# Kernel tuning notes

Measured on AMD Instinct MI355X. Metric: run time of the kernel, lower is better.

The kernel has to match this reference:

```python
import jax, jax.numpy as jnp
import numpy as np

# ---- LIF constants (LIFParams defaults assumed; see notes) ----
SLOPE = 5.0      # surrogate_slope from module
TAU = 20.0
V_REST = -65.0
V_RESET = -65.0
V_TH = -50.0
DT = 1.0

@jax.custom_vjp
def spike(x):
    return (x >= 0).astype(x.dtype)

def _spike_fwd(x):
    return spike(x), x

def _spike_bwd(x, g):
    # fast-sigmoid surrogate gradient
    return (g / (SLOPE * jnp.abs(x) + 1.0) ** 2,)

spike.defvjp(_spike_fwd, _spike_bwd)

def lif_step(v, cur):
    v_new = v + (DT / TAU) * ((V_REST - v) + cur)
    s = spike(v_new - V_TH)
    v_out = v_new - s * (v_new - V_RESET)  # soft reset, grad flows via surrogate
    return v_out, s


def setup_inputs() -> dict:
    key = jax.random.key(0)
    ks = jax.random.split(key, 6)
    B, T = 128, 256
    sizes = [1024, 1024, 1024, 512, 256, 128]  # n_input, hidden..., n_output
    out = {}
    for i in range(5):
        out[f"w{i}"] = jax.random.uniform(ks[i], (sizes[i], sizes[i + 1]), dtype=jnp.float32) * 0.1
    out["input_spikes"] = (jax.random.uniform(ks[5], (B, sizes[0], T)) < 0.2).astype(jnp.float32)
    return out


def _forward(input_spikes, w_layers):
    B, n_in, T = input_spikes.shape
    hidden = [w.shape[1] for w in w_layers[:-1]]
    n_out = w_layers[-1].shape[1]
    dtype = input_spikes.dtype

    # precompute input current for all timesteps: (T, B, H0)
    cur_in = jnp.einsum('bit,ih->tbh', input_spikes, jax.nn.relu(w_layers[0]))
    rws = [jax.nn.relu(w) for w in w_layers[1:]]  # hidden->hidden..., ->output

    v_init = tuple(jnp.full((B, h), V_REST, dtype=dtype) for h in hidden)
    s_init = tuple(jnp.zeros((B, h), dtype=dtype) for h in hidden)
    vo_init = jnp.full((B, n_out), V_REST, dtype=dtype)

    n_hidden = len(hidden)

    def step(carry, cur0):
        vs, vo, sp = carry
        new_vs, new_s = [], []
        v0, s0 = lif_step(vs[0], cur0)
        new_vs.append(v0); new_s.append(s0)
        for li in range(1, n_hidden):
            c = sp[li - 1] @ rws[li - 1]
            v, s = lif_step(vs[li], c)
            new_vs.append(v); new_s.append(s)
        co = sp[-1] @ rws[-1]          # output driven by previous-step spikes
        vo2, so = lif_step(vo, co)
        return (tuple(new_vs), vo2, tuple(new_s)), (tuple(new_s), so)

    _, (hid_T, out_T) = jax.lax.scan(step, (v_init, vo_init, s_init), cur_in)
    hidden_spikes = [jnp.transpose(h, (1, 2, 0)) for h in hid_T]   # (B, h, T)
    output_spikes = jnp.transpose(out_T, (1, 2, 0))                # (B, n_out, T)
    firing_rates = output_spikes.mean(axis=2)
    return hidden_spikes, output_spikes, firing_rates


def reference(input_spikes, w0, w1, w2, w3, w4):
    hidden_spikes, output_spikes, firing_rates = _forward(input_spikes, [w0, w1, w2, w3, w4])
    return (*hidden_spikes, output_spikes, firing_rates)
```

## Files before the change

kernel.cpp:

```cpp
#include <hip/hip_runtime.h>
#include <cstdint>

using u16 = unsigned short;
using u32 = unsigned int;
typedef __attribute__((ext_vector_type(8))) short bhalf8;
typedef __attribute__((ext_vector_type(4))) float floatx4;

__device__ __forceinline__ float bf2f(u16 u) {
  union { unsigned int i; float f; } v; v.i = ((unsigned int)u) << 16; return v.f;
}
__device__ __forceinline__ u16 f2bf(float f) {
  union { float f; unsigned int i; } v; v.f = f;
  unsigned int r = v.i + 0x7fffu + ((v.i >> 16) & 1u);
  return (u16)(r >> 16);
}

__device__ __forceinline__ void gload16(const void* g, void* l) {
  __builtin_amdgcn_global_load_lds((const __attribute__((address_space(1))) void*)g,
                                   (__attribute__((address_space(3))) void*)l, 16, 0, 0);
}

__global__ __launch_bounds__(256) void prep_all(
    const float* __restrict__ w0, const float* __restrict__ w1,
    const float* __restrict__ w2, const float* __restrict__ w3,
    const float* __restrict__ w4, const float* __restrict__ sp,
    u16* __restrict__ W0, u16* __restrict__ W1, u16* __restrict__ W2,
    u16* __restrict__ W3, u16* __restrict__ W4, u16* __restrict__ S,
    u32* __restrict__ flags) {
  const int bid = blockIdx.x;
  const int tid = threadIdx.x;
  const int tx = tid & 31, ty = tid >> 5;
  __shared__ float tile[32][33];

  if (bid == 2720) {
    if (tid < 64) flags[tid] = 0u;
    return;
  }
  if (bid > 2720) {
    const int rel = bid - 2721;
    const int b  = rel >> 8;
    const int i0 = ((rel >> 3) & 31) * 32;
    const int t0 = (rel & 7) * 32;
    const size_t I = 1024, T = 256;
#pragma unroll
    for (int r = 0; r < 4; ++r)
      tile[ty + r * 8][tx] = sp[((size_t)b * I + i0 + ty + r * 8) * T + t0 + tx];
    __syncthreads();
#pragma unroll
    for (int r = 0; r < 4; ++r)
      S[((size_t)(t0 + ty + r * 8) * 128 + b) * I + i0 + tx] = f2bf(tile[tx][ty + r * 8]);
    return;
  }

  const float* W; u16* Wt; int K, N, rel;
  if (bid < 1024)      { W = w0; Wt = W0; K = 1024; N = 1024; rel = bid; }
  else if (bid < 2048) { W = w1; Wt = W1; K = 1024; N = 1024; rel = bid - 1024; }
  else if (bid < 2560) { W = w2; Wt = W2; K = 1024; N =  512; rel = bid - 2048; }
  else if (bid < 2688) { W = w3; Wt = W3; K =  512; N =  256; rel = bid - 2560; }
  else                 { W = w4; Wt = W4; K =  256; N =  128; rel = bid - 2688; }
  const int nx = K >> 5;
  const int k0 = (rel % nx) * 32;
  const int n0 = (rel / nx) * 32;
#pragma unroll
  for (int r = 0; r < 4; ++r)
    tile[ty + r * 8][tx] = W[(size_t)(k0 + ty + r * 8) * N + n0 + tx];
  __syncthreads();
#pragma unroll
  for (int r = 0; r < 4; ++r)
    Wt[(size_t)(n0 + ty + r * 8) * K + k0 + tx] = f2bf(fmaxf(tile[tx][ty + r * 8], 0.f));
}

__global__ __launch_bounds__(256) void gemm_bf16(const u16* __restrict__ A,
                                                 const u16* __restrict__ Bt,
                                                 u16* __restrict__ C,
                                                 int K, int N,
                                                 const u32* __restrict__ flags) {
  __shared__ __align__(16) u16 As[128][64];
  __shared__ __align__(16) u16 Bs[128][64];
  const int tid  = threadIdx.x;
  const int lane = tid & 63;
  const int wave = tid >> 6;
  const int nTn  = N >> 7;
  const int chunk = (256 * nTn) >> 3;
  const int swz   = ((int)blockIdx.x & 7) * chunk + ((int)blockIdx.x >> 3);
  const int mt    = swz / nTn;
  const int nt    = swz - mt * nTn;

  if (flags && (((flags[mt >> 5] >> (mt & 31)) & 1u) == 0u)) return;

  floatx4 acc[4][4];
#pragma unroll
  for (int i = 0; i < 4; ++i)
#pragma unroll
    for (int j = 0; j < 4; ++j)
      acc[i][j] = (floatx4){0.f, 0.f, 0.f, 0.f};

  const int wm = (wave >> 1) * 64;
  const int wn = (wave & 1) * 64;
  const int fr = lane & 15;
  const int fg = lane >> 4;

  const int r_l = lane >> 3;
  const int c_l = (lane & 7) ^ r_l;

  const u16* gA = A  + (size_t)(mt * 128) * K;
  const u16* gB = Bt + (size_t)(nt * 128) * K;

  for (int kt = 0; kt < K; kt += 64) {
#pragma unroll
    for (int q = 0; q < 4; ++q) {
      const int rb0 = (wave * 4 + q) * 8;
      const int rt  = rb0 + r_l;
      gload16(gA + (size_t)rt * K + kt + c_l * 8, &As[rb0][0]);
      gload16(gB + (size_t)rt * K + kt + c_l * 8, &Bs[rb0][0]);
    }
    __syncthreads();

#pragma unroll
    for (int kk = 0; kk < 2; ++kk) {
      bhalf8 af[4], bf[4];
#pragma unroll
      for (int i = 0; i < 4; ++i) {
        const int ra = wm + i * 16 + fr;
        const int rb = wn + i * 16 + fr;
        af[i] = *(const bhalf8*)(&As[ra][((((kk << 2) | fg) ^ (ra & 7)) << 3)]);
        bf[i] = *(const bhalf8*)(&Bs[rb][((((kk << 2) | fg) ^ (rb & 7)) << 3)]);
      }
#pragma unroll
      for (int i = 0; i < 4; ++i)
#pragma unroll
        for (int j = 0; j < 4; ++j)
          acc[i][j] = __builtin_amdgcn_mfma_f32_16x16x32_bf16(af[i], bf[j], acc[i][j], 0, 0, 0);
    }
    __syncthreads();
  }

  const size_t rbase = (size_t)(mt * 128 + wm + fg * 4);
  const size_t cbase = (size_t)(nt * 128 + wn + fr);
#pragma unroll
  for (int i = 0; i < 4; ++i)
#pragma unroll
    for (int j = 0; j < 4; ++j)
#pragma unroll
      for (int r = 0; r < 4; ++r)
        C[(rbase + i * 16 + r) * (size_t)N + cbase + j * 16] = f2bf(acc[i][j][r]);
}

__global__ __launch_bounds__(256) void lif_scan(const u16* __restrict__ Cur,
                                                const u32* __restrict__ aflag,
                                                float* __restrict__ out,
                                                u16* __restrict__ sshift,
                                                u32* __restrict__ oflag,
                                                float* __restrict__ rates,
                                                int H) {
  const int gidx = blockIdx.x * 256 + threadIdx.x;
  const size_t BH = (size_t)128 * H;
  u32 fw[8];
  u32 any = 0;
#pragma unroll
  for (int w = 0; w < 8; ++w) {
    fw[w] = aflag ? aflag[w] : 0xffffffffu;
    any |= fw[w];
  }

  if (any == 0u) {
    const float4 z = {0.f, 0.f, 0.f, 0.f};
    float* base = out + (size_t)blockIdx.x * 65536 + threadIdx.x * 4;
#pragma unroll
    for (int k = 0; k < 64; ++k)
      *(float4*)(base + (size_t)k * 1024) = z;
    if (rates) rates[gidx] = 0.f;
    return;
  }

  float v = -65.f;
  float ssum = 0.f;
  if (sshift) sshift[gidx] = 0;
  float buf[16];
  for (int t0 = 0; t0 < 256; t0 += 16) {
    u32 wavemask = 0;
#pragma unroll
    for (int j = 0; j < 16; ++j) {
      const int t = t0 + j;
      const bool act = ((fw[t >> 5] >> (t & 31)) & 1u) != 0u;
      const float c  = act ? bf2f(Cur[(size_t)t * BH + gidx]) : 0.f;
      const float vn = v + 0.05f * ((-65.f - v) + c);
      const float s  = (vn >= -50.f) ? 1.f : 0.f;
      v = vn - s * (vn + 65.f);
      ssum += s;
      buf[j] = s;
      if (sshift && t < 255)
        sshift[(size_t)(t + 1) * BH + gidx] = (u16)((s != 0.f) ? 0x3F80u : 0u);
      if (oflag) {
        if (__ballot(s != 0.f) != 0ull) wavemask |= (1u << j);
      }
    }
    if (t0 == 240) wavemask &= 0x7fffu;
    if (oflag && wavemask && ((threadIdx.x & 63) == 0)) {
      const unsigned long long m = (unsigned long long)wavemask << ((t0 + 1) & 31);
      const int w = (t0 + 1) >> 5;
      if ((u32)m) atomicOr(&oflag[w], (u32)m);
      if (m >> 32) atomicOr(&oflag[w + 1], (u32)(m >> 32));
    }
    float* o = out + (size_t)gidx * 256 + t0;
#pragma unroll
    for (int q = 0; q < 4; ++q) {
      float4 wv;
      wv.x = buf[q * 4 + 0]; wv.y = buf[q * 4 + 1];
      wv.z = buf[q * 4 + 2]; wv.w = buf[q * 4 + 3];
      *(float4*)(o + q * 4) = wv;
    }
  }
  if (rates) rates[gidx] = ssum * (1.f / 256.f);
}

extern "C" void kernel_launch(void* const* d_in, const int* in_sizes, int n_in,
                              void* d_out, int out_size, void* d_ws, size_t ws_size,
                              hipStream_t stream) {
  const float* w0 = (const float*)d_in[0];
  const float* w1 = (const float*)d_in[1];
  const float* w2 = (const float*)d_in[2];
  const float* w3 = (const float*)d_in[3];
  const float* w4 = (const float*)d_in[4];
  const float* spikes = (const float*)d_in[5];

  uint8_t* ws = (uint8_t*)d_ws;
  u16* S0 = (u16*)(ws + 0);
  u16* S1 = (u16*)(ws + 67108864);
  u16* Cb = (u16*)(ws + 134217728);
  u16* W0 = (u16*)(ws + 201326592);
  u16* W1 = (u16*)(ws + 203423744);
  u16* W2 = (u16*)(ws + 205520896);
  u16* W3 = (u16*)(ws + 206569472);
  u16* W4 = (u16*)(ws + 206831616);
  u32* FL = (u32*)(ws + 206897152);
  u32* F1 = FL +  0;
  u32* F2 = FL + 16;
  u32* F3 = FL + 32;
  u32* F4 = FL + 48;

  float* out0  = (float*)d_out;
  float* out1  = out0 + 33554432;
  float* out2  = out0 + 67108864;
  float* out3  = out0 + 83886080;
  float* out4  = out0 + 92274688;
  float* rates = out0 + 96468992;

  prep_all<<<2721 + 32768, 256, 0, stream>>>(w0, w1, w2, w3, w4, spikes,
                                             W0, W1, W2, W3, W4, S0, FL);

  gemm_bf16<<<256 * 8, 256, 0, stream>>>(S0, W0, Cb, 1024, 1024, nullptr);
  lif_scan<<<512, 256, 0, stream>>>(Cb, nullptr, out0, S1, F1, nullptr, 1024);

  gemm_bf16<<<256 * 8, 256, 0, stream>>>(S1, W1, Cb, 1024, 1024, F1);
  lif_scan<<<512, 256, 0, stream>>>(Cb, F1, out1, S0, F2, nullptr, 1024);

  gemm_bf16<<<256 * 4, 256, 0, stream>>>(S0, W2, Cb, 1024, 512, F2);
  lif_scan<<<256, 256, 0, stream>>>(Cb, F2, out2, S1, F3, nullptr, 512);

  gemm_bf16<<<256 * 2, 256, 0, stream>>>(S1, W3, Cb, 512, 256, F3);
  lif_scan<<<128, 256, 0, stream>>>(Cb, F3, out3, S0, F4, nullptr, 256);

  gemm_bf16<<<256 * 1, 256, 0, stream>>>(S0, W4, Cb, 256, 128, F4);
  lif_scan<<<64, 256, 0, stream>>>(Cb, F4, out4, nullptr, nullptr, rates, 128);
}
```

Measured before the change: 752.4 us.

## Bit-pack spikes in LIF scan and write fp32 outputs coalesced via LDS

The LIF scan now keeps each thread's 256 spikes as eight 32-bit words instead of writing a float4 strip per 16 steps, where each thread wrote to its own strided 1KB row. After the scan, the words go through shared memory so groups of lanes write contiguous 128-byte segments of the (B,H,T) float output, and firing rates come from popcount. The input-spike transpose in prep now uses float4 loads and ushort4 stores. This adds an LDS buffer and a barrier, and fully unrolls the 256-step loop, which may raise register pressure and code size.

```diff
diff --git a/kernel.cpp b/kernel.cpp
--- a/kernel.cpp
+++ b/kernel.cpp
@@ -29,7 +29,6 @@
     u32* __restrict__ flags) {
   const int bid = blockIdx.x;
   const int tid = threadIdx.x;
-  const int tx = tid & 31, ty = tid >> 5;
   __shared__ float tile[32][33];
 
   if (bid == 2720) {
@@ -42,16 +41,28 @@
     const int i0 = ((rel >> 3) & 31) * 32;
     const int t0 = (rel & 7) * 32;
     const size_t I = 1024, T = 256;
-#pragma unroll
-    for (int r = 0; r < 4; ++r)
-      tile[ty + r * 8][tx] = sp[((size_t)b * I + i0 + ty + r * 8) * T + t0 + tx];
+    {
+      const int r  = tid >> 3;
+      const int c4 = (tid & 7) * 4;
+      const float4 v = *(const float4*)(sp + ((size_t)b * I + i0 + r) * T + t0 + c4);
+      tile[r][c4 + 0] = v.x; tile[r][c4 + 1] = v.y;
+      tile[r][c4 + 2] = v.z; tile[r][c4 + 3] = v.w;
+    }
     __syncthreads();
-#pragma unroll
-    for (int r = 0; r < 4; ++r)
-      S[((size_t)(t0 + ty + r * 8) * 128 + b) * I + i0 + tx] = f2bf(tile[tx][ty + r * 8]);
+    {
+      const int tr = tid >> 3;
+      const int ic = (tid & 7) * 4;
+      ushort4 o;
+      o.x = f2bf(tile[ic + 0][tr]);
+      o.y = f2bf(tile[ic + 1][tr]);
+      o.z = f2bf(tile[ic + 2][tr]);
+      o.w = f2bf(tile[ic + 3][tr]);
+      *(ushort4*)(&S[((size_t)(t0 + tr) * 128 + b) * I + i0 + ic]) = o;
+    }
     return;
   }
 
+  const int tx = tid & 31, ty = tid >> 5;
   const float* W; u16* Wt; int K, N, rel;
   if (bid < 1024)      { W = w0; Wt = W0; K = 1024; N = 1024; rel = bid; }
   else if (bid < 2048) { W = w1; Wt = W1; K = 1024; N = 1024; rel = bid - 1024; }
@@ -153,7 +164,8 @@
                                                 u32* __restrict__ oflag,
                                                 float* __restrict__ rates,
                                                 int H) {
-  const int gidx = blockIdx.x * 256 + threadIdx.x;
+  const int tid  = threadIdx.x;
+  const int gidx = blockIdx.x * 256 + tid;
   const size_t BH = (size_t)128 * H;
   u32 fw[8];
   u32 any = 0;
@@ -165,8 +177,7 @@
 
   if (any == 0u) {
     const float4 z = {0.f, 0.f, 0.f, 0.f};
-    float* base = out + (size_t)blockIdx.x * 65536 + threadIdx.x * 4;
-#pragma unroll
+    float* base = out + (size_t)blockIdx.x * 65536 + tid * 4;
     for (int k = 0; k < 64; ++k)
       *(float4*)(base + (size_t)k * 1024) = z;
     if (rates) rates[gidx] = 0.f;
@@ -174,44 +185,63 @@
   }
 
   float v = -65.f;
-  float ssum = 0.f;
+  u32 spk[8];
   if (sshift) sshift[gidx] = 0;
-  float buf[16];
-  for (int t0 = 0; t0 < 256; t0 += 16) {
-    u32 wavemask = 0;
-#pragma unroll
-    for (int j = 0; j < 16; ++j) {
+#pragma unroll
+  for (int t0c = 0; t0c < 8; ++t0c) {
+    const int t0 = t0c * 32;
+    u32 word = 0, cmask = 0;
+#pragma unroll
+    for (int j = 0; j < 32; ++j) {
       const int t = t0 + j;
       const bool act = ((fw[t >> 5] >> (t & 31)) & 1u) != 0u;
-      const float c  = act ? bf2f(Cur[(size_t)t * BH + gidx]) : 0.f;
-      const float vn = v + 0.05f * ((-65.f - v) + c);
-      const float s  = (vn >= -50.f) ? 1.f : 0.f;
-      v = vn - s * (vn + 65.f);
-      ssum += s;
-      buf[j] = s;
+      const float cc = act ? bf2f(Cur[(size_t)t * BH + gidx]) : 0.f;
+      const float vn = v + 0.05f * ((-65.f - v) + cc);
+      const u32 sb = (vn >= -50.f) ? 1u : 0u;
+      v = sb ? -65.f : vn;
+      word |= sb << j;
       if (sshift && t < 255)
-        sshift[(size_t)(t + 1) * BH + gidx] = (u16)((s != 0.f) ? 0x3F80u : 0u);
+        sshift[(size_t)(t + 1) * BH + gidx] = (u16)(sb ? 0x3F80u : 0u);
       if (oflag) {
-        if (__ballot(s != 0.f) != 0ull) wavemask |= (1u << j);
+        if (__ballot(sb != 0u) != 0ull) cmask |= (1u << j);
       }
     }
-    if (t0 == 240) wavemask &= 0x7fffu;
-    if (oflag && wavemask && ((threadIdx.x & 63) == 0)) {
-      const unsigned long long m = (unsigned long long)wavemask << ((t0 + 1) & 31);
-      const int w = (t0 + 1) >> 5;
-      if ((u32)m) atomicOr(&oflag[w], (u32)m);
-      if (m >> 32) atomicOr(&oflag[w + 1], (u32)(m >> 32));
-    }
-    float* o = out + (size_t)gidx * 256 + t0;
-#pragma unroll
-    for (int q = 0; q < 4; ++q) {
-      float4 wv;
-      wv.x = buf[q * 4 + 0]; wv.y = buf[q * 4 + 1];
-      wv.z = buf[q * 4 + 2]; wv.w = buf[q * 4 + 3];
-      *(float4*)(o + q * 4) = wv;
-    }
-  }
-  if (rates) rates[gidx] = ssum * (1.f / 256.f);
+    spk[t0c] = word;
+    if (oflag) {
+      const u32 cm = (t0c == 7) ? (cmask & 0x7fffffffu) : cmask;
+      if (cm && ((tid & 63) == 0)) {
+        const unsigned long long m = (unsigned long long)cm << 1;
+        atomicOr(&oflag[t0c], (u32)m);
+        if ((u32)(m >> 32)) atomicOr(&oflag[t0c + 1], (u32)(m >> 32));
+      }
+    }
+  }
+  if (rates) {
+    int cnt = 0;
+#pragma unroll
+    for (int c = 0; c < 8; ++c) cnt += __popc(spk[c]);
+    rates[gidx] = (float)cnt * (1.f / 256.f);
+  }
+
+  __shared__ u32 lds[256 * 9];
+#pragma unroll
+  for (int c = 0; c < 8; ++c) lds[tid * 9 + c] = spk[c];
+  __syncthreads();
+  const int wv  = tid >> 6, ln = tid & 63;
+  const int grp = ln >> 3;
+  const int sub = ln & 7;
+  float* ob = out + (size_t)blockIdx.x * 65536;
+  for (int rr = 0; rr < 64; rr += 8) {
+    const int row = wv * 64 + rr + grp;
+#pragma unroll
+    for (int c = 0; c < 8; ++c) {
+      const u32 wb = lds[row * 9 + c] >> (sub * 4);
+      float4 f;
+      f.x = (float)(wb & 1u); f.y = (float)((wb >> 1) & 1u);
+      f.z = (float)((wb >> 2) & 1u); f.w = (float)((wb >> 3) & 1u);
+      *(float4*)(ob + (size_t)row * 256 + c * 32 + sub * 4) = f;
+    }
+  }
 }
 
 extern "C" void kernel_launch(void* const* d_in, const int* in_sizes, int n_in,
```

Result: faster. 684.7 us (-9.0%).
